# Kernel tuning notes

Hardware: AMD Instinct MI355X
Metric: run time of the kernel (lower is better)

The kernel has to match this reference:

```python
import jax, jax.numpy as jnp
import numpy as np

N, E = 100000, 1000000
IN_DIM, OUT_DIM, HEADS = 64, 64, 4
C = OUT_DIM // HEADS  # per-head channels = 16
NEG_SLOPE = 0.2
SOFTMAX_EPS = 1e-16  # PyG softmax denominator epsilon
LN_EPS = 1e-5


def setup_inputs() -> dict:
    key = jax.random.key(0)
    ks = jax.random.split(key, 8)
    node_input = jax.random.normal(ks[0], (N, IN_DIM), dtype=jnp.float32)
    edge_index = jax.random.randint(ks[1], (2, E), 0, N, dtype=jnp.int64)
    # GATConv params (glorot-ish scale)
    W = jax.random.normal(ks[2], (IN_DIM, HEADS * C), dtype=jnp.float32) / np.sqrt(IN_DIM)
    att_src = jax.random.normal(ks[3], (HEADS, C), dtype=jnp.float32) / np.sqrt(C)
    att_dst = jax.random.normal(ks[4], (HEADS, C), dtype=jnp.float32) / np.sqrt(C)
    bias = jnp.zeros((HEADS * C,), dtype=jnp.float32)
    # LayerNorm params
    gamma = jnp.ones((OUT_DIM,), dtype=jnp.float32)
    beta = jnp.zeros((OUT_DIM,), dtype=jnp.float32)
    return {"node_input": node_input, "edge_index": edge_index, "W": W,
            "att_src": att_src, "att_dst": att_dst, "bias": bias,
            "gamma": gamma, "beta": beta}


def _gat_forward(x, edge_index, W, att_src, att_dst, bias, gamma, beta):
    src, dst = edge_index[0], edge_index[1]  # message flows src -> dst
    h = (x @ W).reshape(N, HEADS, C)                       # [N, H, C]
    a_src = jnp.einsum('nhc,hc->nh', h, att_src)           # [N, H]
    a_dst = jnp.einsum('nhc,hc->nh', h, att_dst)           # [N, H]
    # per-edge attention logits + leaky relu
    e = a_src[src] + a_dst[dst]                            # [E, H]
    e = jnp.where(e >= 0, e, NEG_SLOPE * e)
    # segment softmax over incoming edges of each target node
    m = jax.ops.segment_max(e, dst, num_segments=N)        # [N, H]
    m = jnp.where(jnp.isfinite(m), m, 0.0)                 # empty segments -> 0
    ex = jnp.exp(e - m[dst])                               # [E, H]
    denom = jax.ops.segment_sum(ex, dst, num_segments=N)   # [N, H]
    alpha = ex / (denom[dst] + SOFTMAX_EPS)                # [E, H]
    # weighted scatter-sum of source features
    msg = alpha[:, :, None] * h[src]                       # [E, H, C]
    out = jax.ops.segment_sum(msg, dst, num_segments=N)    # [N, H, C]
    out = out.reshape(N, HEADS * C) + bias                 # concat heads + bias
    # LayerNorm
    mu = out.mean(axis=-1, keepdims=True)
    var = out.var(axis=-1, keepdims=True)
    out = (out - mu) * jax.lax.rsqrt(var + LN_EPS) * gamma + beta
    # query gate is dead code (graph is a dict -> hasattr fails); dropout is eval identity
    return out


def reference(node_input, edge_index, W, att_src, att_dst, bias, gamma, beta):
    return _gat_forward(node_input, edge_index, W, att_src, att_dst, bias, gamma, beta)
```

## Files before the change

kernel.cpp:

```cpp
#include <hip/hip_runtime.h>
#include <hip/hip_bf16.h>
#include <math.h>

#define N_NODES 100000
#define E_EDGES 1000000
#define HEADS 4
#define DIM 64
#define NEG_SLOPE 0.2f
#define SM_EPS 1e-16f
#define LN_EPS 1e-5f
#define P1_BLOCKS 256
#define NT16 6250
#define GEMM_BLOCKS 1563
#define CHUNK 3907
#define BUCKET_W 512
#define NBUCK 196
#define MAXE2 8

typedef __attribute__((ext_vector_type(8))) short short8v;
typedef __attribute__((ext_vector_type(4))) float f32x4;

static __device__ __forceinline__ unsigned short bfh(float f) {
    __hip_bfloat16 b = __float2bfloat16(f);
    return *reinterpret_cast<unsigned short*>(&b);
}
static __device__ __forceinline__ float bfh2f(unsigned short u) {
    return __uint_as_float((unsigned)u << 16);
}

__global__ __launch_bounds__(256) void k_wprep(
        const float* __restrict__ W, uint4* __restrict__ Wf) {
    int t = threadIdx.x;
    for (int e = t; e < 1024; e += 256) {
        int l = e & 63, f = e >> 6;
        int s = f & 1, kh = (f >> 1) & 1, n = f >> 2;
        int c = n * 16 + (l & 15);
        int k0 = kh * 32 + (l >> 4) * 8;
        unsigned short hw[8];
#pragma unroll
        for (int j = 0; j < 8; ++j) {
            float wv = W[(k0 + j) * 64 + c];
            unsigned short hi = bfh(wv);
            hw[j] = s ? bfh(wv - bfh2f(hi)) : hi;
        }
        uint4 pk;
        pk.x = hw[0] | ((unsigned)hw[1] << 16);
        pk.y = hw[2] | ((unsigned)hw[3] << 16);
        pk.z = hw[4] | ((unsigned)hw[5] << 16);
        pk.w = hw[6] | ((unsigned)hw[7] << 16);
        Wf[e] = pk;
    }
}

__global__ __launch_bounds__(1024) void k_bin(
        const int* __restrict__ ei,
        int2* __restrict__ chunkbuf, int* __restrict__ pre) {
    __shared__ __align__(16) int2 out2[CHUNK];
    __shared__ int cnt[256];
    __shared__ int scan[256];
    int t = threadIdx.x;
    int base_e = blockIdx.x * CHUNK;
    int es[4], ed[4];
#pragma unroll
    for (int k = 0; k < 4; ++k) {
        int i = k * 1024 + t;
        int e = base_e + i;
        bool v = (i < CHUNK) && (e < E_EDGES);
        es[k] = v ? ei[e] : 0;
        ed[k] = v ? ei[E_EDGES + e] : -1;
    }
    if (t < 256) cnt[t] = 0;
    __syncthreads();
#pragma unroll
    for (int k = 0; k < 4; ++k)
        if (ed[k] >= 0) atomicAdd(&cnt[ed[k] >> 9], 1);
    __syncthreads();
    if (t < 256) scan[t] = (t < NBUCK) ? cnt[t] : 0;
    __syncthreads();
#pragma unroll
    for (int off = 1; off < 256; off <<= 1) {
        int v = (t >= off && t < 256) ? scan[t - off] : 0;
        __syncthreads();
        if (t < 256) scan[t] += v;
        __syncthreads();
    }
    if (t < 256) {
        int excl = (t == 0) ? 0 : scan[t - 1];
        if (t < NBUCK) pre[blockIdx.x * (NBUCK + 1) + t] = excl;
        if (t == 0)    pre[blockIdx.x * (NBUCK + 1) + NBUCK] = scan[NBUCK - 1];
        if (t < NBUCK) cnt[t] = excl;
    }
    __syncthreads();
#pragma unroll
    for (int k = 0; k < 4; ++k)
        if (ed[k] >= 0) {
            int pos = atomicAdd(&cnt[ed[k] >> 9], 1);
            out2[pos] = make_int2(es[k], ed[k]);
        }
    __syncthreads();
    int ec = E_EDGES - base_e; ec = (ec > CHUNK) ? CHUNK : ec;
    for (int i = t; i < ec; i += 1024)
        chunkbuf[base_e + i] = out2[i];
}

__global__ __launch_bounds__(256) void k_gemm(
        const float* __restrict__ x, const float* __restrict__ Wf_,
        const float* __restrict__ att_src, const float* __restrict__ att_dst,
        __hip_bfloat16* __restrict__ hb,
        float* __restrict__ asrc, float* __restrict__ adst) {
    int t = threadIdx.x;
    int w = t >> 6, lane = t & 63;
    int tile = blockIdx.x * 4 + w;
    if (tile >= NT16) return;
    int base = tile * 16;
    int m = lane & 15, kg = lane >> 4;

    const float* xr = x + (size_t)(base + m) * 64 + kg * 8;
    short8v ah[2], al[2];
#pragma unroll
    for (int kh = 0; kh < 2; ++kh) {
        float4 q0 = *(const float4*)(xr + kh * 32);
        float4 q1 = *(const float4*)(xr + kh * 32 + 4);
        float qq[8] = {q0.x, q0.y, q0.z, q0.w, q1.x, q1.y, q1.z, q1.w};
#pragma unroll
        for (int j = 0; j < 8; ++j) {
            unsigned short h = bfh(qq[j]);
            ah[kh][j] = (short)h;
            al[kh][j] = (short)bfh(qq[j] - bfh2f(h));
        }
    }

    const short8v* Wfv = (const short8v*)Wf_;
    float vs_keep = 0.f, vd_keep = 0.f;
#pragma unroll
    for (int n = 0; n < 4; ++n) {
        short8v bh0 = Wfv[((n * 2 + 0) * 2 + 0) * 64 + lane];
        short8v bl0 = Wfv[((n * 2 + 0) * 2 + 1) * 64 + lane];
        short8v bh1 = Wfv[((n * 2 + 1) * 2 + 0) * 64 + lane];
        short8v bl1 = Wfv[((n * 2 + 1) * 2 + 1) * 64 + lane];
        f32x4 a4 = {0.f, 0.f, 0.f, 0.f};
        a4 = __builtin_amdgcn_mfma_f32_16x16x32_bf16(ah[0], bh0, a4, 0, 0, 0);
        a4 = __builtin_amdgcn_mfma_f32_16x16x32_bf16(al[0], bh0, a4, 0, 0, 0);
        a4 = __builtin_amdgcn_mfma_f32_16x16x32_bf16(ah[0], bl0, a4, 0, 0, 0);
        a4 = __builtin_amdgcn_mfma_f32_16x16x32_bf16(ah[1], bh1, a4, 0, 0, 0);
        a4 = __builtin_amdgcn_mfma_f32_16x16x32_bf16(al[1], bh1, a4, 0, 0, 0);
        a4 = __builtin_amdgcn_mfma_f32_16x16x32_bf16(ah[1], bl1, a4, 0, 0, 0);
        float asv = att_src[n * 16 + m];
        float adv = att_dst[n * 16 + m];
#pragma unroll
        for (int ri = 0; ri < 4; ++ri) {
            int orow = base + kg * 4 + ri;
            hb[(size_t)orow * 64 + n * 16 + m] = __float2bfloat16(a4[ri]);
            float p = a4[ri] * asv, pd = a4[ri] * adv;
#pragma unroll
            for (int off = 1; off < 16; off <<= 1) {
                p  += __shfl_xor(p,  off, 64);
                pd += __shfl_xor(pd, off, 64);
            }
            if (m == ri * 4 + n) { vs_keep = p; vd_keep = pd; }
        }
    }
    asrc[tile * 64 + kg * 16 + m] = vs_keep;
    adst[tile * 64 + kg * 16 + m] = vd_keep;
}

__global__ __launch_bounds__(1024) void k_bin2(
        const int2* __restrict__ chunkbuf, const int* __restrict__ pre,
        int* __restrict__ cursorP, int* __restrict__ srclist) {
    __shared__ int cnt2[BUCKET_W];
    __shared__ int segstart[P1_BLOCKS];
    __shared__ int segpre[P1_BLOCKS + 1];
    __shared__ int scan[P1_BLOCKS];
    int t = threadIdx.x;
    int b = blockIdx.x;
    int nbase = b * BUCKET_W;
    if (t < BUCKET_W) cnt2[t] = 0;
    int p0 = 0, p1 = 0;
    if (t < 256) {
        p0 = pre[t * (NBUCK + 1) + b];
        p1 = pre[t * (NBUCK + 1) + b + 1];
        segstart[t] = t * CHUNK + p0;
        scan[t] = p0;
    }
    __syncthreads();
#pragma unroll
    for (int off = 128; off >= 1; off >>= 1) {
        int v = (t < off) ? scan[t + off] : 0;
        __syncthreads();
        if (t < off) scan[t] += v;
        __syncthreads();
    }
    int gbase = scan[0];
    __syncthreads();
    if (t < 256) scan[t] = p1 - p0;
    __syncthreads();
#pragma unroll
    for (int off = 1; off < 256; off <<= 1) {
        int v = (t >= off && t < 256) ? scan[t - off] : 0;
        __syncthreads();
        if (t < 256) scan[t] += v;
        __syncthreads();
    }
    if (t < 256) segpre[t + 1] = scan[t];
    if (t == 0) segpre[0] = 0;
    __syncthreads();
    int total = segpre[P1_BLOCKS];
    int2 ecache[MAXE2];
#pragma unroll
    for (int ii = 0; ii < MAXE2; ++ii) {
        int i = ii * 1024 + t;
        if (i < total) {
            int lo = 0, hi = P1_BLOCKS;
#pragma unroll
            for (int it = 0; it < 8; ++it) {
                int mid = (lo + hi) >> 1;
                if (segpre[mid] <= i) lo = mid; else hi = mid;
            }
            int2 e = chunkbuf[segstart[lo] + (i - segpre[lo])];
            ecache[ii] = e;
            atomicAdd(&cnt2[e.y - nbase], 1);
        }
    }
    for (int i = MAXE2 * 1024 + t; i < total; i += 1024) {
        int lo = 0, hi = P1_BLOCKS;
#pragma unroll
        for (int it = 0; it < 8; ++it) {
            int mid = (lo + hi) >> 1;
            if (segpre[mid] <= i) lo = mid; else hi = mid;
        }
        int2 e = chunkbuf[segstart[lo] + (i - segpre[lo])];
        atomicAdd(&cnt2[e.y - nbase], 1);
    }
    __syncthreads();
    int c0 = 0, c1 = 0;
    if (t < 256) {
        c0 = cnt2[2 * t]; c1 = cnt2[2 * t + 1];
        scan[t] = c0 + c1;
    }
    __syncthreads();
#pragma unroll
    for (int off = 1; off < 256; off <<= 1) {
        int v = (t >= off && t < 256) ? scan[t - off] : 0;
        __syncthreads();
        if (t < 256) scan[t] += v;
        __syncthreads();
    }
    if (t < 256) {
        int pexcl = (t == 0) ? 0 : scan[t - 1];
        cnt2[2 * t]     = pexcl;
        cnt2[2 * t + 1] = pexcl + c0;
        int n0 = nbase + 2 * t;
        if (n0 < N_NODES)     cursorP[n0]     = ((gbase + pexcl) << 6) | c0;
        if (n0 + 1 < N_NODES) cursorP[n0 + 1] = ((gbase + pexcl + c0) << 6) | c1;
    }
    __syncthreads();
#pragma unroll
    for (int ii = 0; ii < MAXE2; ++ii) {
        int i = ii * 1024 + t;
        if (i < total) {
            int2 e = ecache[ii];
            int pos = atomicAdd(&cnt2[e.y - nbase], 1);
            srclist[gbase + pos] = e.x;
        }
    }
    for (int i = MAXE2 * 1024 + t; i < total; i += 1024) {
        int lo = 0, hi = P1_BLOCKS;
#pragma unroll
        for (int it = 0; it < 8; ++it) {
            int mid = (lo + hi) >> 1;
            if (segpre[mid] <= i) lo = mid; else hi = mid;
        }
        int2 e = chunkbuf[segstart[lo] + (i - segpre[lo])];
        int pos = atomicAdd(&cnt2[e.y - nbase], 1);
        srclist[gbase + pos] = e.x;
    }
}

__global__ __launch_bounds__(256) void k_aggr(
        const int* __restrict__ cursorP, const int* __restrict__ srclist,
        const float* __restrict__ asrc, const float* __restrict__ adst,
        const __hip_bfloat16* __restrict__ hb,
        const float* __restrict__ bias, const float* __restrict__ gamma,
        const float* __restrict__ beta, float* __restrict__ out) {
    int t = threadIdx.x;
    int lane = t & 63;
    int s = lane >> 5, qq = (lane >> 4) & 1, j = lane & 15;
    int hd = j >> 2;
    int node = blockIdx.x * 8 + (t >> 6) * 2 + s;
    int cw = cursorP[node];
    int dcnt = cw & 63;
    const int* sl = srclist + ((unsigned)cw >> 6);
    int dmax = max(dcnt, __shfl_xor(dcnt, 32, 64));
    const ushort4* hp = (const ushort4*)hb;
    float ad = adst[node * HEADS + hd];
    float acc0 = 0.f, acc1 = 0.f, acc2 = 0.f, acc3 = 0.f, l = 0.f;

    for (int i0 = 0; i0 < dmax; i0 += 8) {
        int idx[4];
        float as[4];
        ushort4 hv[4];
#pragma unroll
        for (int k = 0; k < 4; ++k) {
            int ek = i0 + 2 * k + qq;
            idx[k] = (ek < dcnt) ? sl[ek] : 0;
        }
#pragma unroll
        for (int k = 0; k < 4; ++k) as[k] = asrc[idx[k] * HEADS + hd];
#pragma unroll
        for (int k = 0; k < 4; ++k) hv[k] = hp[idx[k] * 16 + j];
#pragma unroll
        for (int k = 0; k < 4; ++k) {
            int ek = i0 + 2 * k + qq;
            float e = as[k] + ad;
            e = (e >= 0.f) ? e : NEG_SLOPE * e;
            float p = (ek < dcnt) ? __expf(e) : 0.f;
            l += p;
            acc0 += p * __uint_as_float((unsigned)hv[k].x << 16);
            acc1 += p * __uint_as_float((unsigned)hv[k].y << 16);
            acc2 += p * __uint_as_float((unsigned)hv[k].z << 16);
            acc3 += p * __uint_as_float((unsigned)hv[k].w << 16);
        }
    }
    acc0 += __shfl_xor(acc0, 16, 64);
    acc1 += __shfl_xor(acc1, 16, 64);
    acc2 += __shfl_xor(acc2, 16, 64);
    acc3 += __shfl_xor(acc3, 16, 64);
    l    += __shfl_xor(l,    16, 64);

    float inv = 1.f / (l + SM_EPS);
    float4 b4 = ((const float4*)bias)[j];
    float v0 = acc0 * inv + b4.x;
    float v1 = acc1 * inv + b4.y;
    float v2 = acc2 * inv + b4.z;
    float v3 = acc3 * inv + b4.w;
    float s1 = (v0 + v1) + (v2 + v3);
    float s2 = (v0 * v0 + v1 * v1) + (v2 * v2 + v3 * v3);
#pragma unroll
    for (int off = 1; off < 16; off <<= 1) {
        s1 += __shfl_xor(s1, off, 64);
        s2 += __shfl_xor(s2, off, 64);
    }
    float mu = s1 * (1.f / 64.f);
    float var = s2 * (1.f / 64.f) - mu * mu;
    float r = rsqrtf(var + LN_EPS);
    if (qq == 0) {
        float4 g4 = ((const float4*)gamma)[j];
        float4 be4 = ((const float4*)beta)[j];
        float4 o;
        o.x = (v0 - mu) * r * g4.x + be4.x;
        o.y = (v1 - mu) * r * g4.y + be4.y;
        o.z = (v2 - mu) * r * g4.z + be4.z;
        o.w = (v3 - mu) * r * g4.w + be4.w;
        ((float4*)(out + (size_t)node * DIM))[j] = o;
    }
}

extern "C" void kernel_launch(void* const* d_in, const int* in_sizes, int n_in,
                              void* d_out, int out_size, void* d_ws, size_t ws_size,
                              hipStream_t stream) {
    const float* x       = (const float*)d_in[0];
    const int*   ei      = (const int*)d_in[1];
    const float* W       = (const float*)d_in[2];
    const float* att_src = (const float*)d_in[3];
    const float* att_dst = (const float*)d_in[4];
    const float* bias    = (const float*)d_in[5];
    const float* gamma   = (const float*)d_in[6];
    const float* beta    = (const float*)d_in[7];
    float* out = (float*)d_out;

    int2* chunkbuf = (int2*)d_ws;
    int*  pre      = (int*)(chunkbuf + (size_t)P1_BLOCKS * CHUNK);
    int*  cursorP  = pre + (size_t)P1_BLOCKS * (NBUCK + 1);
    int*  srclist  = cursorP + N_NODES;
    float* asrc    = (float*)(srclist + (size_t)E_EDGES);
    float* adst    = asrc + (size_t)N_NODES * HEADS;
    __hip_bfloat16* hb = (__hip_bfloat16*)(adst + (size_t)N_NODES * HEADS);
    uint4* Wf      = (uint4*)(hb + (size_t)N_NODES * DIM);

    k_wprep<<<1, 256, 0, stream>>>(W, Wf);
    k_bin<<<P1_BLOCKS, 1024, 0, stream>>>(ei, chunkbuf, pre);
    k_gemm<<<GEMM_BLOCKS, 256, 0, stream>>>(x, (const float*)Wf, att_src,
                                            att_dst, hb, asrc, adst);
    k_bin2<<<NBUCK, 1024, 0, stream>>>(chunkbuf, pre, cursorP, srclist);
    k_aggr<<<N_NODES / 8, 256, 0, stream>>>(cursorP, srclist, asrc, adst, hb,
                                            bias, gamma, beta, out);
}
```

Before: 156.1 us.

## Fuse weight prep, edge binning and feature GEMM into one launch

Measured after the change: 148.8 us. -4.7%, faster.

```diff
diff --git a/kernel.cpp b/kernel.cpp
--- a/kernel.cpp
+++ b/kernel.cpp
@@ -11,8 +11,10 @@
 #define LN_EPS 1e-5f
 #define P1_BLOCKS 256
 #define NT16 6250
-#define GEMM_BLOCKS 1563
+#define GEMM_BLOCKS 782
+#define K1_BLOCKS (P1_BLOCKS + GEMM_BLOCKS)
 #define CHUNK 3907
+#define EPT 8
 #define BUCKET_W 512
 #define NBUCK 196
 #define MAXE2 8
@@ -28,10 +30,66 @@
     return __uint_as_float((unsigned)u << 16);
 }
 
-__global__ __launch_bounds__(256) void k_wprep(
-        const float* __restrict__ W, uint4* __restrict__ Wf) {
+__global__ __launch_bounds__(512) void k_feat(
+        const float* __restrict__ x, const float* __restrict__ W,
+        const float* __restrict__ att_src, const float* __restrict__ att_dst,
+        const int* __restrict__ ei, __hip_bfloat16* __restrict__ hb,
+        float* __restrict__ asrc, float* __restrict__ adst,
+        int2* __restrict__ chunkbuf, int* __restrict__ pre) {
+    __shared__ __align__(16) int smem_i[8326];
     int t = threadIdx.x;
-    for (int e = t; e < 1024; e += 256) {
+
+    if (blockIdx.x < P1_BLOCKS) {
+        int2* out2 = (int2*)smem_i;
+        int*  cnt  = smem_i + 2 * CHUNK;
+        int*  scan = cnt + 256;
+        int base_e = blockIdx.x * CHUNK;
+        int es[EPT], ed[EPT];
+#pragma unroll
+        for (int k = 0; k < EPT; ++k) {
+            int i = k * 512 + t;
+            int e = base_e + i;
+            bool v = (i < CHUNK) && (e < E_EDGES);
+            es[k] = v ? ei[e] : 0;
+            ed[k] = v ? ei[E_EDGES + e] : -1;
+        }
+        if (t < 256) cnt[t] = 0;
+        __syncthreads();
+#pragma unroll
+        for (int k = 0; k < EPT; ++k)
+            if (ed[k] >= 0) atomicAdd(&cnt[ed[k] >> 9], 1);
+        __syncthreads();
+        if (t < 256) scan[t] = (t < NBUCK) ? cnt[t] : 0;
+        __syncthreads();
+#pragma unroll
+        for (int off = 1; off < 256; off <<= 1) {
+            int v = (t >= off && t < 256) ? scan[t - off] : 0;
+            __syncthreads();
+            if (t < 256) scan[t] += v;
+            __syncthreads();
+        }
+        if (t < 256) {
+            int excl = (t == 0) ? 0 : scan[t - 1];
+            if (t < NBUCK) pre[blockIdx.x * (NBUCK + 1) + t] = excl;
+            if (t == 0)    pre[blockIdx.x * (NBUCK + 1) + NBUCK] = scan[NBUCK - 1];
+            if (t < NBUCK) cnt[t] = excl;
+        }
+        __syncthreads();
+#pragma unroll
+        for (int k = 0; k < EPT; ++k)
+            if (ed[k] >= 0) {
+                int pos = atomicAdd(&cnt[ed[k] >> 9], 1);
+                out2[pos] = make_int2(es[k], ed[k]);
+            }
+        __syncthreads();
+        int ec = E_EDGES - base_e; ec = (ec > CHUNK) ? CHUNK : ec;
+        for (int i = t; i < ec; i += 512)
+            chunkbuf[base_e + i] = out2[i];
+        return;
+    }
+
+    uint4* Wlds = (uint4*)smem_i;
+    for (int e = t; e < 1024; e += 512) {
         int l = e & 63, f = e >> 6;
         int s = f & 1, kh = (f >> 1) & 1, n = f >> 2;
         int c = n * 16 + (l & 15);
@@ -48,69 +106,12 @@
         pk.y = hw[2] | ((unsigned)hw[3] << 16);
         pk.z = hw[4] | ((unsigned)hw[5] << 16);
         pk.w = hw[6] | ((unsigned)hw[7] << 16);
-        Wf[e] = pk;
-    }
-}
-
-__global__ __launch_bounds__(1024) void k_bin(
-        const int* __restrict__ ei,
-        int2* __restrict__ chunkbuf, int* __restrict__ pre) {
-    __shared__ __align__(16) int2 out2[CHUNK];
-    __shared__ int cnt[256];
-    __shared__ int scan[256];
-    int t = threadIdx.x;
-    int base_e = blockIdx.x * CHUNK;
-    int es[4], ed[4];
-#pragma unroll
-    for (int k = 0; k < 4; ++k) {
-        int i = k * 1024 + t;
-        int e = base_e + i;
-        bool v = (i < CHUNK) && (e < E_EDGES);
-        es[k] = v ? ei[e] : 0;
-        ed[k] = v ? ei[E_EDGES + e] : -1;
-    }
-    if (t < 256) cnt[t] = 0;
-    __syncthreads();
-#pragma unroll
-    for (int k = 0; k < 4; ++k)
-        if (ed[k] >= 0) atomicAdd(&cnt[ed[k] >> 9], 1);
-    __syncthreads();
-    if (t < 256) scan[t] = (t < NBUCK) ? cnt[t] : 0;
-    __syncthreads();
-#pragma unroll
-    for (int off = 1; off < 256; off <<= 1) {
-        int v = (t >= off && t < 256) ? scan[t - off] : 0;
-        __syncthreads();
-        if (t < 256) scan[t] += v;
-        __syncthreads();
-    }
-    if (t < 256) {
-        int excl = (t == 0) ? 0 : scan[t - 1];
-        if (t < NBUCK) pre[blockIdx.x * (NBUCK + 1) + t] = excl;
-        if (t == 0)    pre[blockIdx.x * (NBUCK + 1) + NBUCK] = scan[NBUCK - 1];
-        if (t < NBUCK) cnt[t] = excl;
-    }
-    __syncthreads();
-#pragma unroll
-    for (int k = 0; k < 4; ++k)
-        if (ed[k] >= 0) {
-            int pos = atomicAdd(&cnt[ed[k] >> 9], 1);
-            out2[pos] = make_int2(es[k], ed[k]);
-        }
-    __syncthreads();
-    int ec = E_EDGES - base_e; ec = (ec > CHUNK) ? CHUNK : ec;
-    for (int i = t; i < ec; i += 1024)
-        chunkbuf[base_e + i] = out2[i];
-}
-
-__global__ __launch_bounds__(256) void k_gemm(
-        const float* __restrict__ x, const float* __restrict__ Wf_,
-        const float* __restrict__ att_src, const float* __restrict__ att_dst,
-        __hip_bfloat16* __restrict__ hb,
-        float* __restrict__ asrc, float* __restrict__ adst) {
-    int t = threadIdx.x;
+        Wlds[e] = pk;
+    }
+    __syncthreads();
+
     int w = t >> 6, lane = t & 63;
-    int tile = blockIdx.x * 4 + w;
+    int tile = (blockIdx.x - P1_BLOCKS) * 8 + w;
     if (tile >= NT16) return;
     int base = tile * 16;
     int m = lane & 15, kg = lane >> 4;
@@ -130,7 +131,7 @@
         }
     }
 
-    const short8v* Wfv = (const short8v*)Wf_;
+    const short8v* Wfv = (const short8v*)Wlds;
     float vs_keep = 0.f, vd_keep = 0.f;
 #pragma unroll
     for (int n = 0; n < 4; ++n) {
@@ -375,12 +376,9 @@
     float* asrc    = (float*)(srclist + (size_t)E_EDGES);
     float* adst    = asrc + (size_t)N_NODES * HEADS;
     __hip_bfloat16* hb = (__hip_bfloat16*)(adst + (size_t)N_NODES * HEADS);
-    uint4* Wf      = (uint4*)(hb + (size_t)N_NODES * DIM);
-
-    k_wprep<<<1, 256, 0, stream>>>(W, Wf);
-    k_bin<<<P1_BLOCKS, 1024, 0, stream>>>(ei, chunkbuf, pre);
-    k_gemm<<<GEMM_BLOCKS, 256, 0, stream>>>(x, (const float*)Wf, att_src,
-                                            att_dst, hb, asrc, adst);
+
+    k_feat<<<K1_BLOCKS, 512, 0, stream>>>(x, W, att_src, att_dst, ei,
+                                          hb, asrc, adst, chunkbuf, pre);
     k_bin2<<<NBUCK, 1024, 0, stream>>>(chunkbuf, pre, cursorP, srclist);
     k_aggr<<<N_NODES / 8, 256, 0, stream>>>(cursorP, srclist, asrc, adst, hb,
                                             bias, gamma, beta, out);
```
